# Optimization experiments

Measured on AMD Instinct MI355X. Metric: run time of the kernel, lower is better.

Reference implementation:

```python
import jax, jax.numpy as jnp
import numpy as np

H = 1024   # hidden_size
NH = 16    # num_heads
HD = H // NH
B, S = 2, 2048


def setup_inputs() -> dict:
    key = jax.random.key(0)
    ks = jax.random.split(key, 6)
    std = 0.02
    x = jax.random.normal(ks[0], (B, S, H), dtype=jnp.float32)
    w_qkv = jax.random.normal(ks[1], (3 * H, H), dtype=jnp.float32) * std
    b_qkv = jnp.zeros((3 * H,), dtype=jnp.float32)
    ln_g = jnp.ones((H,), dtype=jnp.float32)
    ln_b = jnp.zeros((H,), dtype=jnp.float32)
    w_ent = jax.random.normal(ks[2], (1, H), dtype=jnp.float32) * std
    b_ent = jnp.zeros((1,), dtype=jnp.float32)
    w_out = jax.random.normal(ks[3], (H, H), dtype=jnp.float32) * std
    b_out = jnp.zeros((H,), dtype=jnp.float32)
    return {"x": x, "ln_g": ln_g, "ln_b": ln_b, "w_qkv": w_qkv, "b_qkv": b_qkv,
            "w_ent": w_ent, "b_ent": b_ent, "w_out": w_out, "b_out": b_out}


def reference(x, ln_g, ln_b, w_qkv, b_qkv, w_ent, b_ent, w_out, b_out):
    b, s, h = x.shape
    scale = 1.0 / jnp.sqrt(jnp.float32(HD))
    TEMP = 0.1  # fixed softmax temperature

    # LayerNorm (eps=1e-6)
    mu = jnp.mean(x, axis=-1, keepdims=True)
    var = jnp.mean(jnp.square(x - mu), axis=-1, keepdims=True)
    xn = (x - mu) / jnp.sqrt(var + 1e-6) * ln_g + ln_b

    # QKV projection -> [B, S, 3, NH, HD] -> q,k,v each [B, NH, S, HD]
    qkv = xn @ w_qkv.T + b_qkv
    qkv = qkv.reshape(b, s, 3, NH, HD).transpose(2, 0, 3, 1, 4)
    q, k, v = qkv[0], qkv[1], qkv[2]

    # Scaled causal scores [B, NH, S, S]
    scores = jnp.einsum('bhqd,bhkd->bhqk', q, k) * scale
    causal = jnp.tril(jnp.ones((s, s), dtype=bool))
    scores = jnp.where(causal[None, None], scores, -jnp.inf)

    # Sharpened softmax (temperature 0.1); dropout is identity in eval
    probs = jax.nn.softmax(scores / TEMP, axis=-1)

    # Entropy gate over keys: sigmoid proj on post-LN x, clamped [0.1, 2.0]
    gate = jax.nn.sigmoid(xn @ w_ent.T + b_ent)        # [B, S, 1]
    gate = jnp.clip(gate, 0.1, 2.0)[:, None, None, :, 0]  # [B, 1, 1, S]
    probs = probs * gate

    # Weighted values -> merge heads -> output projection, scaled by 0.1
    out = jnp.einsum('bhqk,bhkd->bhqd', probs, v)
    out = out.transpose(0, 2, 1, 3).reshape(b, s, h)
    return (out @ w_out.T + b_out) * 0.1
```

## Files before the change

kernel.cpp:

```cpp
#include <hip/hip_runtime.h>

typedef __bf16 bf16x8 __attribute__((ext_vector_type(8)));
typedef float floatx4 __attribute__((ext_vector_type(4)));
typedef unsigned short u16;

#define LOG2E 1.44269504088896340736f
#define BF16_ONE 0x3F80u

static __device__ __forceinline__ float bf2f(u16 u) {
  union { unsigned int i; float f; } c; c.i = ((unsigned int)u) << 16; return c.f;
}
static __device__ __forceinline__ u16 f2bf(float f) {
  union { float f; unsigned int i; } c; c.f = f;
  unsigned int x = c.i;
  unsigned int r = (x >> 16) & 1u;
  x += 0x7fffu + r;
  return (u16)(x >> 16);
}
static __device__ __forceinline__ u16 f2bf_rne(float f) {
  __bf16 h = (__bf16)f;
  union { __bf16 h; u16 u; } c; c.h = h; return c.u;
}
static __device__ __forceinline__ float fast_exp2(float x) {
#if __has_builtin(__builtin_amdgcn_exp2f)
  return __builtin_amdgcn_exp2f(x);
#else
  return exp2f(x);
#endif
}
static __device__ __forceinline__ float ldp(const void* p, int i, bool isbf) {
  return isbf ? bf2f(((const u16*)p)[i]) : ((const float*)p)[i];
}

static __device__ __forceinline__ float blockSum(float v, float* red, int wave, int lane) {
  #pragma unroll
  for (int o = 32; o > 0; o >>= 1) v += __shfl_xor(v, o);
  __syncthreads();
  if (lane == 0) red[wave] = v;
  __syncthreads();
  return red[0] + red[1] + red[2] + red[3];
}

__global__ __launch_bounds__(256) void prep_kernel(
    const void* __restrict__ w_qkv, u16* __restrict__ w_qkv_c,
    const void* __restrict__ w_out, u16* __restrict__ w_out_c,
    const void* __restrict__ x, const void* __restrict__ g, const void* __restrict__ bta,
    const void* __restrict__ w_ent, const void* __restrict__ b_ent,
    u16* __restrict__ xn, float* __restrict__ gate, const u16* __restrict__ probe)
{
  __shared__ float red[4];
  bool isbf = (probe[0] == BF16_ONE);
  int blk = blockIdx.x;
  int tid = threadIdx.x;

  if (blk < 2048) {
    int i = blk * 256 + tid;
    const void* src = w_qkv; u16* dst = w_qkv_c;
    if (i >= 393216) { i -= 393216; src = w_out; dst = w_out_c; }
    if (isbf) {
      ((uint4*)dst)[i] = ((const uint4*)src)[i];
    } else {
      const float4* s = (const float4*)src;
      float4 a = s[2 * i], b = s[2 * i + 1];
      u16 o[8] = {f2bf(a.x), f2bf(a.y), f2bf(a.z), f2bf(a.w),
                  f2bf(b.x), f2bf(b.y), f2bf(b.z), f2bf(b.w)};
      *(uint4*)(&dst[8 * i]) = *(uint4*)o;
    }
    return;
  }

  int row = blk - 2048;
  int wave = tid >> 6, lane = tid & 63;

  float v[4];
  #pragma unroll
  for (int i = 0; i < 4; ++i) {
    size_t idx = (size_t)row * 1024 + tid + 256 * i;
    v[i] = isbf ? bf2f(((const u16*)x)[idx]) : ((const float*)x)[idx];
  }

  float mu = blockSum(v[0] + v[1] + v[2] + v[3], red, wave, lane) * (1.0f / 1024.0f);

  float vs = 0.f;
  #pragma unroll
  for (int i = 0; i < 4; ++i) { float d = v[i] - mu; vs += d * d; }
  float var = blockSum(vs, red, wave, lane) * (1.0f / 1024.0f);
  float rstd = rsqrtf(var + 1e-6f);

  float gp = 0.f;
  #pragma unroll
  for (int i = 0; i < 4; ++i) {
    int col = tid + 256 * i;
    float xv = (v[i] - mu) * rstd * ldp(g, col, isbf) + ldp(bta, col, isbf);
    xn[(size_t)row * 1024 + col] = f2bf(xv);
    gp += xv * ldp(w_ent, col, isbf);
  }
  float tot = blockSum(gp, red, wave, lane);
  if (tid == 0) {
    float z = tot + ldp(b_ent, 0, isbf);
    float sg = 1.0f / (1.0f + exp2f(-z * LOG2E));
    gate[row] = fminf(fmaxf(sg, 0.1f), 2.0f);
  }
}

#define GEMM_STAGE(Abase, Wbase) \
  { \
    int lrow = lane >> 3; \
    int scb = ((lane & 7) ^ lrow) * 8; \
    _Pragma("unroll") \
    for (int it = 0; it < 4; ++it) { \
      int chunk = wave * 4 + it; \
      int row = chunk * 8 + lrow; \
      __builtin_amdgcn_global_load_lds( \
        (const __attribute__((address_space(1))) void*)&Abase[(size_t)(m0 + row) * K + k0 + scb], \
        (__attribute__((address_space(3))) void*)&As[chunk * 512], 16, 0, 0); \
      __builtin_amdgcn_global_load_lds( \
        (const __attribute__((address_space(1))) void*)&Wbase[(size_t)(n0 + row) * K + k0 + scb], \
        (__attribute__((address_space(3))) void*)&Ws[chunk * 512], 16, 0, 0); \
    } \
  }

#define GEMM_COMPUTE() \
  _Pragma("unroll") \
  for (int kk = 0; kk < 64; kk += 32) { \
    int kkb = kk >> 3; \
    bf16x8 af[4], bfr[4]; \
    _Pragma("unroll") \
    for (int i = 0; i < 4; ++i) \
      af[i] = *(const bf16x8*)(&As[(wm + 16 * i + lr) * 64 + ((kkb + lg) ^ (lr & 7)) * 8]); \
    _Pragma("unroll") \
    for (int j = 0; j < 4; ++j) \
      bfr[j] = *(const bf16x8*)(&Ws[(wn + 16 * j + lr) * 64 + ((kkb + lg) ^ (lr & 7)) * 8]); \
    _Pragma("unroll") \
    for (int i = 0; i < 4; ++i) \
      _Pragma("unroll") \
      for (int j = 0; j < 4; ++j) \
        acc[i][j] = __builtin_amdgcn_mfma_f32_16x16x32_bf16(af[i], bfr[j], acc[i][j], 0, 0, 0); \
  }

__global__ __launch_bounds__(256) void gemm_bt_kernel(
    const u16* __restrict__ A, const u16* __restrict__ W, const void* __restrict__ bias,
    const float* __restrict__ gate, u16* __restrict__ C, int M, int N, int K,
    const u16* __restrict__ probe)
{
  __shared__ __align__(16) u16 As[128 * 64];
  __shared__ __align__(16) u16 Ws[128 * 64];
  int m0 = blockIdx.y * 128, n0 = blockIdx.x * 128;
  int tid = threadIdx.x, wave = tid >> 6, lane = tid & 63;
  int lr = lane & 15, lg = lane >> 4;
  int wm = (wave >> 1) * 64, wn = (wave & 1) * 64;

  floatx4 acc[4][4];
  #pragma unroll
  for (int i = 0; i < 4; ++i)
    #pragma unroll
    for (int j = 0; j < 4; ++j)
      #pragma unroll
      for (int r = 0; r < 4; ++r) acc[i][j][r] = 0.f;

  for (int k0 = 0; k0 < K; k0 += 64) {
    GEMM_STAGE(A, W)
    __syncthreads();
    GEMM_COMPUTE()
    __syncthreads();
  }

  bool isbf = (probe[0] == BF16_ONE);
  bool doGate = (n0 >= 2048);
  float gm[4][4];
  #pragma unroll
  for (int i = 0; i < 4; ++i)
    #pragma unroll
    for (int r = 0; r < 4; ++r)
      gm[i][r] = doGate ? gate[m0 + wm + 16 * i + lg * 4 + r] : 1.0f;

  #pragma unroll
  for (int j = 0; j < 4; ++j) {
    int n = n0 + wn + 16 * j + lr;
    float bv = ldp(bias, n, isbf);
    #pragma unroll
    for (int i = 0; i < 4; ++i) {
      int mbase = m0 + wm + 16 * i + lg * 4;
      #pragma unroll
      for (int r = 0; r < 4; ++r)
        C[(size_t)(mbase + r) * N + n] = f2bf((acc[i][j][r] + bv) * gm[i][r]);
    }
  }
}

__global__ __launch_bounds__(256) void gemm_out_kernel(
    const u16* __restrict__ A, const u16* __restrict__ W, const void* __restrict__ bias,
    void* __restrict__ C, int M, int N, int K, float scale, const u16* __restrict__ probe)
{
  __shared__ __align__(16) u16 As[64 * 64];
  __shared__ __align__(16) u16 Ws[128 * 64];
  int m0 = blockIdx.y * 64, n0 = blockIdx.x * 128;
  int tid = threadIdx.x, wave = tid >> 6, lane = tid & 63;
  int lr = lane & 15, lg = lane >> 4;
  int wn = wave * 32;

  floatx4 acc[4][2];
  #pragma unroll
  for (int i = 0; i < 4; ++i)
    #pragma unroll
    for (int j = 0; j < 2; ++j)
      #pragma unroll
      for (int r = 0; r < 4; ++r) acc[i][j][r] = 0.f;

  for (int k0 = 0; k0 < K; k0 += 64) {
    {
      int lrow = lane >> 3;
      int scb = ((lane & 7) ^ lrow) * 8;
      #pragma unroll
      for (int c = wave; c < 24; c += 4) {
        if (c < 8) {
          int row = c * 8 + lrow;
          __builtin_amdgcn_global_load_lds(
            (const __attribute__((address_space(1))) void*)&A[(size_t)(m0 + row) * K + k0 + scb],
            (__attribute__((address_space(3))) void*)&As[c * 512], 16, 0, 0);
        } else {
          int cc = c - 8;
          int row = cc * 8 + lrow;
          __builtin_amdgcn_global_load_lds(
            (const __attribute__((address_space(1))) void*)&W[(size_t)(n0 + row) * K + k0 + scb],
            (__attribute__((address_space(3))) void*)&Ws[cc * 512], 16, 0, 0);
        }
      }
    }
    __syncthreads();
    #pragma unroll
    for (int kk = 0; kk < 64; kk += 32) {
      int kkb = kk >> 3;
      bf16x8 af[4], bfr[2];
      #pragma unroll
      for (int i = 0; i < 4; ++i)
        af[i] = *(const bf16x8*)(&As[(16 * i + lr) * 64 + ((kkb + lg) ^ (lr & 7)) * 8]);
      #pragma unroll
      for (int j = 0; j < 2; ++j)
        bfr[j] = *(const bf16x8*)(&Ws[(wn + 16 * j + lr) * 64 + ((kkb + lg) ^ (lr & 7)) * 8]);
      #pragma unroll
      for (int i = 0; i < 4; ++i)
        #pragma unroll
        for (int j = 0; j < 2; ++j)
          acc[i][j] = __builtin_amdgcn_mfma_f32_16x16x32_bf16(af[i], bfr[j], acc[i][j], 0, 0, 0);
    }
    __syncthreads();
  }

  bool isbf = (probe[0] == BF16_ONE);
  #pragma unroll
  for (int j = 0; j < 2; ++j) {
    int n = n0 + wn + 16 * j + lr;
    float bv = ldp(bias, n, isbf);
    #pragma unroll
    for (int i = 0; i < 4; ++i) {
      int mbase = m0 + 16 * i + lg * 4;
      #pragma unroll
      for (int r = 0; r < 4; ++r) {
        float v = (acc[i][j][r] + bv) * scale;
        size_t idx = (size_t)(mbase + r) * N + n;
        if (isbf) ((u16*)C)[idx] = f2bf(v);
        else      ((float*)C)[idx] = v;
      }
    }
  }
}

#define PSTR 72
#define CEXP (1.25f * LOG2E)

static __device__ __forceinline__ void attn_half(
    const u16* __restrict__ Ks, const u16* __restrict__ Vt, u16* __restrict__ ps,
    const bf16x8* qf, floatx4* accO, float& l,
    bool diag, int qg, int lr, int lg)
{
  #pragma unroll
  for (int jt = 0; jt < 4; ++jt) {
    floatx4 a = {0.f, 0.f, 0.f, 0.f};
    __builtin_amdgcn_s_setprio(1);
    #pragma unroll
    for (int kk = 0; kk < 2; ++kk) {
      bf16x8 bk = *(const bf16x8*)(&Ks[(jt * 16 + lr) * 72 + kk * 32 + lg * 8]);
      a = __builtin_amdgcn_mfma_f32_16x16x32_bf16(bk, qf[kk], a, 0, 0, 0);
    }
    __builtin_amdgcn_s_setprio(0);
    int kbase = jt * 16 + lg * 4;
    u16 pb[4];
    #pragma unroll
    for (int r = 0; r < 4; ++r) {
      float e = fast_exp2(a[r] * CEXP);
      if (diag && (kbase + r) > qg) e = 0.f;
      l += e;
      pb[r] = f2bf_rne(e);
    }
    *(uint2*)(&ps[lr * PSTR + kbase]) = *(uint2*)pb;
  }
  bf16x8 ap[2];
  #pragma unroll
  for (int kk = 0; kk < 2; ++kk)
    ap[kk] = *(const bf16x8*)(&ps[lr * PSTR + kk * 32 + lg * 8]);
  __builtin_amdgcn_s_setprio(1);
  #pragma unroll
  for (int jt = 0; jt < 4; ++jt)
    #pragma unroll
    for (int kk = 0; kk < 2; ++kk) {
      bf16x8 bv = *(const bf16x8*)(&Vt[(jt * 16 + lr) * 72 + kk * 32 + lg * 8]);
      accO[jt] = __builtin_amdgcn_mfma_f32_16x16x32_bf16(ap[kk], bv, accO[jt], 0, 0, 0);
    }
  __builtin_amdgcn_s_setprio(0);
}

__global__ __launch_bounds__(256) void attn_kernel(
    const u16* __restrict__ qkv, u16* __restrict__ out)
{
  __shared__ __align__(16) u16 Ks[2][64 * 72];
  __shared__ __align__(16) u16 Vt[2][64 * 72];
  __shared__ __align__(16) u16 Ps[4][16 * PSTR];

  int bid = blockIdx.x;
  int xcd = bid & 7, kb = bid >> 3;
  int bh = xcd * 4 + (kb >> 4);
  int pr = kb & 15;
  int h = bh & 15, b = bh >> 4;
  int tid = threadIdx.x, wave = tid >> 6, lane = tid & 63;
  int lr = lane & 15, lg = lane >> 4;
  const int RS = 3072;

  int tA = pr, tB = 31 - pr;

  bf16x8 qfA[2], qfB[2];
  int qrbA = b * 2048 + tA * 64 + wave * 16;
  int qrbB = b * 2048 + tB * 64 + wave * 16;
  #pragma unroll
  for (int kk = 0; kk < 2; ++kk) {
    qfA[kk] = *(const bf16x8*)(&qkv[(size_t)(qrbA + lr) * RS + h * 64 + kk * 32 + lg * 8]);
    qfB[kk] = *(const bf16x8*)(&qkv[(size_t)(qrbB + lr) * RS + h * 64 + kk * 32 + lg * 8]);
  }

  floatx4 accOA[4], accOB[4];
  float lA = 0.f, lB = 0.f;
  #pragma unroll
  for (int jt = 0; jt < 4; ++jt)
    #pragma unroll
    for (int r = 0; r < 4; ++r) { accOA[jt][r] = 0.f; accOB[jt][r] = 0.f; }

  u16* ps = Ps[wave];

  int srow = tid >> 3, sc8 = (tid & 7) * 8;
  int vkey = tid & 63, vd0 = (tid >> 6) * 16;

  uint4 kp0, kp1, vp0, vp1;

  auto LOADK = [&](int kt) {
    int krow0 = b * 2048 + kt * 64;
    kp0 = *(const uint4*)(&qkv[(size_t)(krow0 + srow) * RS + 1024 + h * 64 + sc8]);
    kp1 = *(const uint4*)(&qkv[(size_t)(krow0 + 32 + srow) * RS + 1024 + h * 64 + sc8]);
    const u16* vrow = &qkv[(size_t)(krow0 + vkey) * RS + 2048 + h * 64 + vd0];
    vp0 = *(const uint4*)(vrow);
    vp1 = *(const uint4*)(vrow + 8);
  };
  auto COMMIT = [&](int bi) {
    u16* ksb = (u16*)Ks[bi];
    u16* vtb = (u16*)Vt[bi];
    *(uint4*)(&ksb[srow * 72 + sc8]) = kp0;
    *(uint4*)(&ksb[(srow + 32) * 72 + sc8]) = kp1;
    unsigned int ww[8] = {vp0.x, vp0.y, vp0.z, vp0.w, vp1.x, vp1.y, vp1.z, vp1.w};
    #pragma unroll
    for (int i = 0; i < 8; ++i) {
      vtb[(vd0 + 2 * i) * 72 + vkey]     = (u16)(ww[i] & 0xffffu);
      vtb[(vd0 + 2 * i + 1) * 72 + vkey] = (u16)(ww[i] >> 16);
    }
  };

  LOADK(0);
  COMMIT(0);
  LOADK(1);
  __syncthreads();

  int qg = wave * 16 + lr;
  for (int kt = 0; kt <= tB; ++kt) {
    int cur = kt & 1;
    bool diagB = (kt == tB), diagA = (kt == tA);
    if (kt <= tA) {
      attn_half(Ks[cur], Vt[cur], ps, qfB, accOB, lB, diagB, qg, lr, lg);
      attn_half(Ks[cur], Vt[cur], ps, qfA, accOA, lA, diagA, qg, lr, lg);
    } else {
      attn_half(Ks[cur], Vt[cur], ps, qfB, accOB, lB, diagB, qg, lr, lg);
    }
    if (kt < tB) {
      COMMIT(cur ^ 1);
      if (kt + 2 <= tB) LOADK(kt + 2);
      __syncthreads();
    }
  }

  lB += __shfl_xor(lB, 16); lB += __shfl_xor(lB, 32);
  lA += __shfl_xor(lA, 16); lA += __shfl_xor(lA, 32);
  float liB[4], liA[4];
  #pragma unroll
  for (int r = 0; r < 4; ++r) {
    liB[r] = 1.0f / fmaxf(__shfl(lB, lg * 4 + r), 1e-30f);
    liA[r] = 1.0f / fmaxf(__shfl(lA, lg * 4 + r), 1e-30f);
  }
  #pragma unroll
  for (int jt = 0; jt < 4; ++jt)
    #pragma unroll
    for (int r = 0; r < 4; ++r) {
      int mB = qrbB + lg * 4 + r;
      out[(size_t)mB * 1024 + h * 64 + jt * 16 + lr] = f2bf(accOB[jt][r] * liB[r]);
      int mA = qrbA + lg * 4 + r;
      out[(size_t)mA * 1024 + h * 64 + jt * 16 + lr] = f2bf(accOA[jt][r] * liA[r]);
    }
}

extern "C" void kernel_launch(void* const* d_in, const int* in_sizes, int n_in,
                              void* d_out, int out_size, void* d_ws, size_t ws_size,
                              hipStream_t stream) {
  const void* x     = d_in[0];
  const void* ln_g  = d_in[1];
  const void* ln_b  = d_in[2];
  const void* w_qkv = d_in[3];
  const void* b_qkv = d_in[4];
  const void* w_ent = d_in[5];
  const void* b_ent = d_in[6];
  const void* w_out = d_in[7];
  const void* b_out = d_in[8];
  const u16* probe = (const u16*)ln_g;

  char* ws = (char*)d_ws;
  float* gate    = (float*)(ws);
  u16* xc        = (u16*)(ws + (64u << 10));
  u16* qkvb      = (u16*)(ws + (64u << 10) + (8u << 20));
  u16* w_qkv_c   = (u16*)(ws + (64u << 10) + (32u << 20));
  u16* w_out_c   = (u16*)(ws + (64u << 10) + (38u << 20));

  prep_kernel<<<6144, 256, 0, stream>>>(w_qkv, w_qkv_c, w_out, w_out_c,
                                        x, ln_g, ln_b, w_ent, b_ent, xc, gate, probe);
  gemm_bt_kernel<<<dim3(24, 32), 256, 0, stream>>>(xc, w_qkv_c, b_qkv, gate, qkvb, 4096, 3072, 1024, probe);
  attn_kernel<<<512, 256, 0, stream>>>(qkvb, xc );
  gemm_out_kernel<<<dim3(8, 64), 256, 0, stream>>>(xc, w_out_c, b_out, d_out, 4096, 1024, 1024, 0.1f, probe);
}
```

Baseline: 207.9 us.

## Load K fragments directly into registers and interleave both query tiles

K tiles are no longer staged through shared memory. Each wave loads its K MFMA fragments straight from global memory into double-buffered registers, and only V goes through LDS, with a new packed transpose that writes 8-byte words. The two query tiles A and B are now processed together in one templated routine with separate P scratch buffers, so their MFMAs and exps interleave and the V fragments read from LDS are reused. The setprio hints are removed. This cuts LDS traffic and exposes more independent work, but adds many registers (16 bf16x8 for K), which may reduce occupancy, and every wave now fetches the whole K tile redundantly from global memory.

```diff
diff --git a/kernel.cpp b/kernel.cpp
--- a/kernel.cpp
+++ b/kernel.cpp
@@ -269,53 +269,62 @@
 #define PSTR 72
 #define CEXP (1.25f * LOG2E)
 
-static __device__ __forceinline__ void attn_half(
-    const u16* __restrict__ Ks, const u16* __restrict__ Vt, u16* __restrict__ ps,
-    const bf16x8* qf, floatx4* accO, float& l,
-    bool diag, int qg, int lr, int lg)
+template<bool DOA>
+static __device__ __forceinline__ void tile_compute(
+    const bf16x8 (&kf)[4][2], const u16* __restrict__ Vtb,
+    u16* __restrict__ psB, u16* __restrict__ psA,
+    const bf16x8* qfB, const bf16x8* qfA,
+    floatx4* accOB, floatx4* accOA, float& lB, float& lA,
+    bool diagB, bool diagA, int qg, int lr, int lg)
 {
   #pragma unroll
   for (int jt = 0; jt < 4; ++jt) {
-    floatx4 a = {0.f, 0.f, 0.f, 0.f};
-    __builtin_amdgcn_s_setprio(1);
+    floatx4 aB = {0.f, 0.f, 0.f, 0.f};
+    floatx4 aA = {0.f, 0.f, 0.f, 0.f};
     #pragma unroll
     for (int kk = 0; kk < 2; ++kk) {
-      bf16x8 bk = *(const bf16x8*)(&Ks[(jt * 16 + lr) * 72 + kk * 32 + lg * 8]);
-      a = __builtin_amdgcn_mfma_f32_16x16x32_bf16(bk, qf[kk], a, 0, 0, 0);
-    }
-    __builtin_amdgcn_s_setprio(0);
+      aB = __builtin_amdgcn_mfma_f32_16x16x32_bf16(kf[jt][kk], qfB[kk], aB, 0, 0, 0);
+      if (DOA) aA = __builtin_amdgcn_mfma_f32_16x16x32_bf16(kf[jt][kk], qfA[kk], aA, 0, 0, 0);
+    }
     int kbase = jt * 16 + lg * 4;
-    u16 pb[4];
+    u16 pb[4], pa[4];
     #pragma unroll
     for (int r = 0; r < 4; ++r) {
-      float e = fast_exp2(a[r] * CEXP);
-      if (diag && (kbase + r) > qg) e = 0.f;
-      l += e;
-      pb[r] = f2bf_rne(e);
-    }
-    *(uint2*)(&ps[lr * PSTR + kbase]) = *(uint2*)pb;
-  }
-  bf16x8 ap[2];
-  #pragma unroll
-  for (int kk = 0; kk < 2; ++kk)
-    ap[kk] = *(const bf16x8*)(&ps[lr * PSTR + kk * 32 + lg * 8]);
-  __builtin_amdgcn_s_setprio(1);
+      float eB = fast_exp2(aB[r] * CEXP);
+      if (diagB && (kbase + r) > qg) eB = 0.f;
+      lB += eB;
+      pb[r] = f2bf_rne(eB);
+      if (DOA) {
+        float eA = fast_exp2(aA[r] * CEXP);
+        if (diagA && (kbase + r) > qg) eA = 0.f;
+        lA += eA;
+        pa[r] = f2bf_rne(eA);
+      }
+    }
+    *(uint2*)(&psB[lr * PSTR + kbase]) = *(uint2*)pb;
+    if (DOA) *(uint2*)(&psA[lr * PSTR + kbase]) = *(uint2*)pa;
+  }
+  bf16x8 apB[2], apA[2];
+  #pragma unroll
+  for (int kk = 0; kk < 2; ++kk) {
+    apB[kk] = *(const bf16x8*)(&psB[lr * PSTR + kk * 32 + lg * 8]);
+    if (DOA) apA[kk] = *(const bf16x8*)(&psA[lr * PSTR + kk * 32 + lg * 8]);
+  }
   #pragma unroll
   for (int jt = 0; jt < 4; ++jt)
     #pragma unroll
     for (int kk = 0; kk < 2; ++kk) {
-      bf16x8 bv = *(const bf16x8*)(&Vt[(jt * 16 + lr) * 72 + kk * 32 + lg * 8]);
-      accO[jt] = __builtin_amdgcn_mfma_f32_16x16x32_bf16(ap[kk], bv, accO[jt], 0, 0, 0);
-    }
-  __builtin_amdgcn_s_setprio(0);
+      bf16x8 bv = *(const bf16x8*)(&Vtb[(jt * 16 + lr) * 72 + kk * 32 + lg * 8]);
+      accOB[jt] = __builtin_amdgcn_mfma_f32_16x16x32_bf16(apB[kk], bv, accOB[jt], 0, 0, 0);
+      if (DOA) accOA[jt] = __builtin_amdgcn_mfma_f32_16x16x32_bf16(apA[kk], bv, accOA[jt], 0, 0, 0);
+    }
 }
 
 __global__ __launch_bounds__(256) void attn_kernel(
     const u16* __restrict__ qkv, u16* __restrict__ out)
 {
-  __shared__ __align__(16) u16 Ks[2][64 * 72];
   __shared__ __align__(16) u16 Vt[2][64 * 72];
-  __shared__ __align__(16) u16 Ps[4][16 * PSTR];
+  __shared__ __align__(16) u16 Ps[8][16 * PSTR];
 
   int bid = blockIdx.x;
   int xcd = bid & 7, kb = bid >> 3;
@@ -344,52 +353,78 @@
     #pragma unroll
     for (int r = 0; r < 4; ++r) { accOA[jt][r] = 0.f; accOB[jt][r] = 0.f; }
 
-  u16* ps = Ps[wave];
-
-  int srow = tid >> 3, sc8 = (tid & 7) * 8;
-  int vkey = tid & 63, vd0 = (tid >> 6) * 16;
-
-  uint4 kp0, kp1, vp0, vp1;
-
-  auto LOADK = [&](int kt) {
-    int krow0 = b * 2048 + kt * 64;
-    kp0 = *(const uint4*)(&qkv[(size_t)(krow0 + srow) * RS + 1024 + h * 64 + sc8]);
-    kp1 = *(const uint4*)(&qkv[(size_t)(krow0 + 32 + srow) * RS + 1024 + h * 64 + sc8]);
-    const u16* vrow = &qkv[(size_t)(krow0 + vkey) * RS + 2048 + h * 64 + vd0];
-    vp0 = *(const uint4*)(vrow);
-    vp1 = *(const uint4*)(vrow + 8);
+  u16* psB = Ps[wave];
+  u16* psA = Ps[4 + wave];
+
+  bf16x8 kf0[4][2], kf1[4][2];
+  auto LOADK = [&](bf16x8 (&kf)[4][2], int kt) {
+    const u16* kbp = &qkv[(size_t)(b * 2048 + kt * 64) * RS + 1024 + h * 64];
+    #pragma unroll
+    for (int jt = 0; jt < 4; ++jt)
+      #pragma unroll
+      for (int kk = 0; kk < 2; ++kk)
+        kf[jt][kk] = *(const bf16x8*)(&kbp[(jt * 16 + lr) * RS + kk * 32 + lg * 8]);
   };
-  auto COMMIT = [&](int bi) {
-    u16* ksb = (u16*)Ks[bi];
+
+  int kq = tid & 15, dg = tid >> 4;
+  uint2 vv[4];
+  auto LOADV = [&](int kt) {
+    const u16* vbp = &qkv[(size_t)(b * 2048 + kt * 64) * RS + 2048 + h * 64];
+    #pragma unroll
+    for (int i = 0; i < 4; ++i)
+      vv[i] = *(const uint2*)(&vbp[(4 * kq + i) * RS + 4 * dg]);
+  };
+  auto COMMITV = [&](int bi) {
     u16* vtb = (u16*)Vt[bi];
-    *(uint4*)(&ksb[srow * 72 + sc8]) = kp0;
-    *(uint4*)(&ksb[(srow + 32) * 72 + sc8]) = kp1;
-    unsigned int ww[8] = {vp0.x, vp0.y, vp0.z, vp0.w, vp1.x, vp1.y, vp1.z, vp1.w};
-    #pragma unroll
-    for (int i = 0; i < 8; ++i) {
-      vtb[(vd0 + 2 * i) * 72 + vkey]     = (u16)(ww[i] & 0xffffu);
-      vtb[(vd0 + 2 * i + 1) * 72 + vkey] = (u16)(ww[i] >> 16);
-    }
+    unsigned lo0 = vv[0].x, lo1 = vv[1].x, lo2 = vv[2].x, lo3 = vv[3].x;
+    unsigned hi0 = vv[0].y, hi1 = vv[1].y, hi2 = vv[2].y, hi3 = vv[3].y;
+    uint2 w0, w1, w2, w3;
+    w0.x = (lo0 & 0xffffu) | (lo1 << 16);
+    w0.y = (lo2 & 0xffffu) | (lo3 << 16);
+    w1.x = (lo0 >> 16) | (lo1 & 0xffff0000u);
+    w1.y = (lo2 >> 16) | (lo3 & 0xffff0000u);
+    w2.x = (hi0 & 0xffffu) | (hi1 << 16);
+    w2.y = (hi2 & 0xffffu) | (hi3 << 16);
+    w3.x = (hi0 >> 16) | (hi1 & 0xffff0000u);
+    w3.y = (hi2 >> 16) | (hi3 & 0xffff0000u);
+    *(uint2*)(&vtb[(4 * dg + 0) * 72 + 4 * kq]) = w0;
+    *(uint2*)(&vtb[(4 * dg + 1) * 72 + 4 * kq]) = w1;
+    *(uint2*)(&vtb[(4 * dg + 2) * 72 + 4 * kq]) = w2;
+    *(uint2*)(&vtb[(4 * dg + 3) * 72 + 4 * kq]) = w3;
   };
 
-  LOADK(0);
-  COMMIT(0);
-  LOADK(1);
+  LOADV(0);
+  LOADK(kf0, 0);
+  COMMITV(0);
+  LOADV(1);
+  LOADK(kf1, 1);
   __syncthreads();
 
   int qg = wave * 16 + lr;
   for (int kt = 0; kt <= tB; ++kt) {
     int cur = kt & 1;
     bool diagB = (kt == tB), diagA = (kt == tA);
-    if (kt <= tA) {
-      attn_half(Ks[cur], Vt[cur], ps, qfB, accOB, lB, diagB, qg, lr, lg);
-      attn_half(Ks[cur], Vt[cur], ps, qfA, accOA, lA, diagA, qg, lr, lg);
+    const u16* vtb = (const u16*)Vt[cur];
+    if (cur == 0) {
+      if (kt <= tA)
+        tile_compute<true >(kf0, vtb, psB, psA, qfB, qfA, accOB, accOA, lB, lA,
+                            diagB, diagA, qg, lr, lg);
+      else
+        tile_compute<false>(kf0, vtb, psB, psA, qfB, qfA, accOB, accOA, lB, lA,
+                            diagB, diagA, qg, lr, lg);
+      if (kt + 2 <= tB) LOADK(kf0, kt + 2);
     } else {
-      attn_half(Ks[cur], Vt[cur], ps, qfB, accOB, lB, diagB, qg, lr, lg);
+      if (kt <= tA)
+        tile_compute<true >(kf1, vtb, psB, psA, qfB, qfA, accOB, accOA, lB, lA,
+                            diagB, diagA, qg, lr, lg);
+      else
+        tile_compute<false>(kf1, vtb, psB, psA, qfB, qfA, accOB, accOA, lB, lA,
+                            diagB, diagA, qg, lr, lg);
+      if (kt + 2 <= tB) LOADK(kf1, kt + 2);
     }
     if (kt < tB) {
-      COMMIT(cur ^ 1);
-      if (kt + 2 <= tB) LOADK(kt + 2);
+      COMMITV(cur ^ 1);
+      if (kt + 2 <= tB) LOADV(kt + 2);
       __syncthreads();
     }
   }
```

Measured after the change: 286.0 us. +37.6%, slower.

## Split paired query tiles across 8 waves and pack V transpose stores

Applied to the files above, without the earlier changes.

The attention block grows from 4 to 8 waves. The first four waves handle the late query tile and the last four handle the early query tile, so each wave keeps one accumulator set instead of two and the tiles run concurrently rather than serially. The K/V staging is redistributed over 512 threads, and the V transpose now writes packed 32-bit pairs instead of 16-bit scalars. The s_setprio hints are dropped. Waves in the A half sit idle once past their tile, and the larger block changes occupancy and register limits.

```diff
diff --git a/kernel.cpp b/kernel.cpp
--- a/kernel.cpp
+++ b/kernel.cpp
@@ -269,53 +269,12 @@
 #define PSTR 72
 #define CEXP (1.25f * LOG2E)
 
-static __device__ __forceinline__ void attn_half(
-    const u16* __restrict__ Ks, const u16* __restrict__ Vt, u16* __restrict__ ps,
-    const bf16x8* qf, floatx4* accO, float& l,
-    bool diag, int qg, int lr, int lg)
-{
-  #pragma unroll
-  for (int jt = 0; jt < 4; ++jt) {
-    floatx4 a = {0.f, 0.f, 0.f, 0.f};
-    __builtin_amdgcn_s_setprio(1);
-    #pragma unroll
-    for (int kk = 0; kk < 2; ++kk) {
-      bf16x8 bk = *(const bf16x8*)(&Ks[(jt * 16 + lr) * 72 + kk * 32 + lg * 8]);
-      a = __builtin_amdgcn_mfma_f32_16x16x32_bf16(bk, qf[kk], a, 0, 0, 0);
-    }
-    __builtin_amdgcn_s_setprio(0);
-    int kbase = jt * 16 + lg * 4;
-    u16 pb[4];
-    #pragma unroll
-    for (int r = 0; r < 4; ++r) {
-      float e = fast_exp2(a[r] * CEXP);
-      if (diag && (kbase + r) > qg) e = 0.f;
-      l += e;
-      pb[r] = f2bf_rne(e);
-    }
-    *(uint2*)(&ps[lr * PSTR + kbase]) = *(uint2*)pb;
-  }
-  bf16x8 ap[2];
-  #pragma unroll
-  for (int kk = 0; kk < 2; ++kk)
-    ap[kk] = *(const bf16x8*)(&ps[lr * PSTR + kk * 32 + lg * 8]);
-  __builtin_amdgcn_s_setprio(1);
-  #pragma unroll
-  for (int jt = 0; jt < 4; ++jt)
-    #pragma unroll
-    for (int kk = 0; kk < 2; ++kk) {
-      bf16x8 bv = *(const bf16x8*)(&Vt[(jt * 16 + lr) * 72 + kk * 32 + lg * 8]);
-      accO[jt] = __builtin_amdgcn_mfma_f32_16x16x32_bf16(ap[kk], bv, accO[jt], 0, 0, 0);
-    }
-  __builtin_amdgcn_s_setprio(0);
-}
-
-__global__ __launch_bounds__(256) void attn_kernel(
+__global__ __launch_bounds__(512, 4) void attn_kernel(
     const u16* __restrict__ qkv, u16* __restrict__ out)
 {
   __shared__ __align__(16) u16 Ks[2][64 * 72];
   __shared__ __align__(16) u16 Vt[2][64 * 72];
-  __shared__ __align__(16) u16 Ps[4][16 * PSTR];
+  __shared__ __align__(16) u16 Ps[8][16 * PSTR];
 
   int bid = blockIdx.x;
   int xcd = bid & 7, kb = bid >> 3;
@@ -327,89 +286,109 @@
   const int RS = 3072;
 
   int tA = pr, tB = 31 - pr;
-
-  bf16x8 qfA[2], qfB[2];
-  int qrbA = b * 2048 + tA * 64 + wave * 16;
-  int qrbB = b * 2048 + tB * 64 + wave * 16;
-  #pragma unroll
-  for (int kk = 0; kk < 2; ++kk) {
-    qfA[kk] = *(const bf16x8*)(&qkv[(size_t)(qrbA + lr) * RS + h * 64 + kk * 32 + lg * 8]);
-    qfB[kk] = *(const bf16x8*)(&qkv[(size_t)(qrbB + lr) * RS + h * 64 + kk * 32 + lg * 8]);
-  }
-
-  floatx4 accOA[4], accOB[4];
-  float lA = 0.f, lB = 0.f;
+  bool isA = (wave >= 4);
+  int wv = wave & 3;
+  int myT = isA ? tA : tB;
+
+  bf16x8 qf[2];
+  int qrb = b * 2048 + myT * 64 + wv * 16;
+  #pragma unroll
+  for (int kk = 0; kk < 2; ++kk)
+    qf[kk] = *(const bf16x8*)(&qkv[(size_t)(qrb + lr) * RS + h * 64 + kk * 32 + lg * 8]);
+
+  floatx4 accO[4];
+  float l = 0.f;
   #pragma unroll
   for (int jt = 0; jt < 4; ++jt)
     #pragma unroll
-    for (int r = 0; r < 4; ++r) { accOA[jt][r] = 0.f; accOB[jt][r] = 0.f; }
+    for (int r = 0; r < 4; ++r) accO[jt][r] = 0.f;
 
   u16* ps = Ps[wave];
 
   int srow = tid >> 3, sc8 = (tid & 7) * 8;
-  int vkey = tid & 63, vd0 = (tid >> 6) * 16;
-
-  uint4 kp0, kp1, vp0, vp1;
-
-  auto LOADK = [&](int kt) {
+  int kq = tid & 31, dg = tid >> 5;
+  uint4 kp;
+  uint2 vv0, vv1;
+
+  auto LOADKV = [&](int kt) {
     int krow0 = b * 2048 + kt * 64;
-    kp0 = *(const uint4*)(&qkv[(size_t)(krow0 + srow) * RS + 1024 + h * 64 + sc8]);
-    kp1 = *(const uint4*)(&qkv[(size_t)(krow0 + 32 + srow) * RS + 1024 + h * 64 + sc8]);
-    const u16* vrow = &qkv[(size_t)(krow0 + vkey) * RS + 2048 + h * 64 + vd0];
-    vp0 = *(const uint4*)(vrow);
-    vp1 = *(const uint4*)(vrow + 8);
+    kp = *(const uint4*)(&qkv[(size_t)(krow0 + srow) * RS + 1024 + h * 64 + sc8]);
+    const u16* vbp = &qkv[(size_t)krow0 * RS + 2048 + h * 64];
+    vv0 = *(const uint2*)(&vbp[(size_t)(2 * kq) * RS + 4 * dg]);
+    vv1 = *(const uint2*)(&vbp[(size_t)(2 * kq + 1) * RS + 4 * dg]);
   };
   auto COMMIT = [&](int bi) {
-    u16* ksb = (u16*)Ks[bi];
-    u16* vtb = (u16*)Vt[bi];
-    *(uint4*)(&ksb[srow * 72 + sc8]) = kp0;
-    *(uint4*)(&ksb[(srow + 32) * 72 + sc8]) = kp1;
-    unsigned int ww[8] = {vp0.x, vp0.y, vp0.z, vp0.w, vp1.x, vp1.y, vp1.z, vp1.w};
-    #pragma unroll
-    for (int i = 0; i < 8; ++i) {
-      vtb[(vd0 + 2 * i) * 72 + vkey]     = (u16)(ww[i] & 0xffffu);
-      vtb[(vd0 + 2 * i + 1) * 72 + vkey] = (u16)(ww[i] >> 16);
+    *(uint4*)(&Ks[bi][srow * 72 + sc8]) = kp;
+    #pragma unroll
+    for (int d = 0; d < 4; ++d) {
+      unsigned w0 = (&vv0.x)[d >> 1], w1 = (&vv1.x)[d >> 1];
+      unsigned e0 = (d & 1) ? (w0 >> 16) : (w0 & 0xffffu);
+      unsigned e1 = (d & 1) ? (w1 >> 16) : (w1 & 0xffffu);
+      *(unsigned*)(&Vt[bi][(4 * dg + d) * 72 + 2 * kq]) = e0 | (e1 << 16);
     }
   };
 
-  LOADK(0);
+  LOADKV(0);
   COMMIT(0);
-  LOADK(1);
+  LOADKV(1);
   __syncthreads();
 
-  int qg = wave * 16 + lr;
+  int qg = wv * 16 + lr;
   for (int kt = 0; kt <= tB; ++kt) {
     int cur = kt & 1;
-    bool diagB = (kt == tB), diagA = (kt == tA);
-    if (kt <= tA) {
-      attn_half(Ks[cur], Vt[cur], ps, qfB, accOB, lB, diagB, qg, lr, lg);
-      attn_half(Ks[cur], Vt[cur], ps, qfA, accOA, lA, diagA, qg, lr, lg);
-    } else {
-      attn_half(Ks[cur], Vt[cur], ps, qfB, accOB, lB, diagB, qg, lr, lg);
+    if (!isA || kt <= tA) {
+      bool diag = (kt == myT);
+      const u16* ks = Ks[cur];
+      const u16* vt = Vt[cur];
+      #pragma unroll
+      for (int jt = 0; jt < 4; ++jt) {
+        floatx4 a = {0.f, 0.f, 0.f, 0.f};
+        #pragma unroll
+        for (int kk = 0; kk < 2; ++kk) {
+          bf16x8 bk = *(const bf16x8*)(&ks[(jt * 16 + lr) * 72 + kk * 32 + lg * 8]);
+          a = __builtin_amdgcn_mfma_f32_16x16x32_bf16(bk, qf[kk], a, 0, 0, 0);
+        }
+        int kbase = jt * 16 + lg * 4;
+        u16 pb[4];
+        #pragma unroll
+        for (int r = 0; r < 4; ++r) {
+          float e = fast_exp2(a[r] * CEXP);
+          if (diag && (kbase + r) > qg) e = 0.f;
+          l += e;
+          pb[r] = f2bf_rne(e);
+        }
+        *(uint2*)(&ps[lr * PSTR + kbase]) = *(uint2*)pb;
+      }
+      bf16x8 ap[2];
+      #pragma unroll
+      for (int kk = 0; kk < 2; ++kk)
+        ap[kk] = *(const bf16x8*)(&ps[lr * PSTR + kk * 32 + lg * 8]);
+      #pragma unroll
+      for (int jt = 0; jt < 4; ++jt)
+        #pragma unroll
+        for (int kk = 0; kk < 2; ++kk) {
+          bf16x8 bv = *(const bf16x8*)(&vt[(jt * 16 + lr) * 72 + kk * 32 + lg * 8]);
+          accO[jt] = __builtin_amdgcn_mfma_f32_16x16x32_bf16(ap[kk], bv, accO[jt], 0, 0, 0);
+        }
     }
     if (kt < tB) {
       COMMIT(cur ^ 1);
-      if (kt + 2 <= tB) LOADK(kt + 2);
+      if (kt + 2 <= tB) LOADKV(kt + 2);
       __syncthreads();
     }
   }
 
-  lB += __shfl_xor(lB, 16); lB += __shfl_xor(lB, 32);
-  lA += __shfl_xor(lA, 16); lA += __shfl_xor(lA, 32);
-  float liB[4], liA[4];
-  #pragma unroll
-  for (int r = 0; r < 4; ++r) {
-    liB[r] = 1.0f / fmaxf(__shfl(lB, lg * 4 + r), 1e-30f);
-    liA[r] = 1.0f / fmaxf(__shfl(lA, lg * 4 + r), 1e-30f);
-  }
+  l += __shfl_xor(l, 16); l += __shfl_xor(l, 32);
+  float li[4];
+  #pragma unroll
+  for (int r = 0; r < 4; ++r)
+    li[r] = 1.0f / fmaxf(__shfl(l, lg * 4 + r), 1e-30f);
   #pragma unroll
   for (int jt = 0; jt < 4; ++jt)
     #pragma unroll
     for (int r = 0; r < 4; ++r) {
-      int mB = qrbB + lg * 4 + r;
-      out[(size_t)mB * 1024 + h * 64 + jt * 16 + lr] = f2bf(accOB[jt][r] * liB[r]);
-      int mA = qrbA + lg * 4 + r;
-      out[(size_t)mA * 1024 + h * 64 + jt * 16 + lr] = f2bf(accOA[jt][r] * liA[r]);
+      int m = qrb + lg * 4 + r;
+      out[(size_t)m * 1024 + h * 64 + jt * 16 + lr] = f2bf(accO[jt][r] * li[r]);
     }
 }
 
@@ -437,6 +416,6 @@
   prep_kernel<<<6144, 256, 0, stream>>>(w_qkv, w_qkv_c, w_out, w_out_c,
                                         x, ln_g, ln_b, w_ent, b_ent, xc, gate, probe);
   gemm_bt_kernel<<<dim3(24, 32), 256, 0, stream>>>(xc, w_qkv_c, b_qkv, gate, qkvb, 4096, 3072, 1024, probe);
-  attn_kernel<<<512, 256, 0, stream>>>(qkvb, xc );
+  attn_kernel<<<512, 512, 0, stream>>>(qkvb, xc );
   gemm_out_kernel<<<dim3(8, 64), 256, 0, stream>>>(xc, w_out_c, b_out, d_out, 4096, 1024, 1024, 0.1f, probe);
 }
```

Measured after the change: 199.0 us. 4.3% less time.
